# Performance work log

Hardware: AMD Instinct MI355X
Metric: run time of the kernel (lower is better)

## Reference

```python
import jax, jax.numpy as jnp
import numpy as np

TEMPERATURE = 0.0005

def conv1d(x, w, b):
    # x: [B,Cin,T], w: [Cout,Cin,K], 'same' padding as ConvNorm (pad=(K-1)//2)
    pad = (w.shape[-1] - 1) // 2
    y = jax.lax.conv_general_dilated(x, w, window_strides=(1,), padding=[(pad, pad)],
                                     dimension_numbers=('NCH', 'OIH', 'NCH'))
    return y + b[None, :, None]

def setup_inputs() -> dict:
    key = jax.random.key(0)
    ks = jax.random.split(key, 20)
    B, C_MEL, C_TXT, C_ATT, T1, T2 = 32, 80, 512, 80, 1600, 400
    s = 0.02
    return {
        'queries': jax.random.normal(ks[0], (B, C_MEL, T1), jnp.float32),
        'keys': jax.random.normal(ks[1], (B, C_TXT, T2), jnp.float32),
        'mask': jax.random.randint(ks[2], (B, T2, 1), 0, 2).astype(bool),
        'attn_prior': jax.random.uniform(ks[3], (B, T1, T2), jnp.float32),
        'speaker_embed': jax.random.normal(ks[4], (B, C_TXT), jnp.float32),
        # key_proj: Conv(512->1024,k3) -> ReLU -> Conv(1024->80,k1)
        'Wk1': jax.random.normal(ks[5], (C_TXT * 2, C_TXT, 3)) * s,
        'bk1': jax.random.normal(ks[6], (C_TXT * 2,)) * s,
        'Wk2': jax.random.normal(ks[7], (C_ATT, C_TXT * 2, 1)) * s,
        'bk2': jax.random.normal(ks[8], (C_ATT,)) * s,
        # query_proj: Conv(80->160,k3) -> ReLU -> Conv(160->80,k1) -> ReLU -> Conv(80->80,k1)
        'Wq1': jax.random.normal(ks[9], (C_MEL * 2, C_MEL, 3)) * s,
        'bq1': jax.random.normal(ks[10], (C_MEL * 2,)) * s,
        'Wq2': jax.random.normal(ks[11], (C_MEL, C_MEL * 2, 1)) * s,
        'bq2': jax.random.normal(ks[12], (C_MEL,)) * s,
        'Wq3': jax.random.normal(ks[13], (C_ATT, C_MEL, 1)) * s,
        'bq3': jax.random.normal(ks[14], (C_ATT,)) * s,
        # speaker projections (multi_speaker=True)
        'Wks': jax.random.normal(ks[15], (C_TXT, C_TXT)) * s,
        'bks': jax.random.normal(ks[16], (C_TXT,)) * s,
        'Wqs': jax.random.normal(ks[17], (C_MEL, C_TXT)) * s,
        'bqs': jax.random.normal(ks[18], (C_MEL,)) * s,
    }

def reference(queries, keys, mask, attn_prior, speaker_embed,
              Wk1, bk1, Wk2, bk2, Wq1, bq1, Wq2, bq2, Wq3, bq3,
              Wks, bks, Wqs, bqs):
    # speaker conditioning: Linear(spk) broadcast over time, added channelwise
    keys = keys + (speaker_embed @ Wks.T + bks)[:, :, None]
    queries = queries + (speaker_embed @ Wqs.T + bqs)[:, :, None]
    # projections
    k = jax.nn.relu(conv1d(keys, Wk1, bk1))
    k = conv1d(k, Wk2, bk2)                      # [B, C_att, T2]
    q = jax.nn.relu(conv1d(queries, Wq1, bq1))
    q = jax.nn.relu(conv1d(q, Wq2, bq2))
    q = conv1d(q, Wq3, bq3)                      # [B, C_att, T1]
    # -temp * sum_c (q-k)^2 == -temp * (||q||^2 + ||k||^2 - 2 q.k)
    q2 = jnp.sum(q * q, axis=1)                  # [B, T1]
    k2 = jnp.sum(k * k, axis=1)                  # [B, T2]
    qk = jnp.einsum('bct,bcs->bts', q, k)        # [B, T1, T2]
    attn = -TEMPERATURE * (q2[:, :, None] + k2[:, None, :] - 2.0 * qk)
    attn = attn[:, None]                         # [B, 1, T1, T2]
    attn = jax.nn.log_softmax(attn, axis=3) + jnp.log(attn_prior[:, None] + 1e-8)
    attn_logprob = attn
    m = jnp.transpose(mask, (0, 2, 1))[:, :, None, :]  # [B,1,1,T2]
    attn = jnp.where(m, -jnp.inf, attn)
    attn = jax.nn.softmax(attn, axis=3)
    return attn, attn_logprob
```

## Files before the change

### kernel.cpp

```cpp
#include <hip/hip_runtime.h>
#include <math.h>

#define TEMP 0.0005f
#define B_    32
#define CMEL  80
#define CTXT  512
#define T1_   1600
#define T2_   400

typedef short short8 __attribute__((ext_vector_type(8)));
typedef float f32x4 __attribute__((ext_vector_type(4)));

__device__ inline unsigned short f2bf(float f) {
    unsigned u = __float_as_uint(f);
    u += 0x7FFF + ((u >> 16) & 1);
    return (unsigned short)(u >> 16);
}
__device__ inline unsigned pack2(float a, float b) {
    return (unsigned)f2bf(a) | ((unsigned)f2bf(b) << 16);
}
__device__ inline float bf2f(unsigned short v) { return __uint_as_float(((unsigned)v) << 16); }

__global__ void bias_kernel(const float* __restrict__ se,
                            const float* __restrict__ Wks, const float* __restrict__ bks,
                            const float* __restrict__ Wqs, const float* __restrict__ bqs,
                            float* __restrict__ kb, float* __restrict__ qb) {
    int tid = blockIdx.x * blockDim.x + threadIdx.x;
    const int nk = B_ * CTXT;
    if (tid < nk) {
        int b = tid / CTXT, c = tid % CTXT;
        const float4* s4 = reinterpret_cast<const float4*>(se + b * CTXT);
        const float4* w4 = reinterpret_cast<const float4*>(Wks + (size_t)c * CTXT);
        float acc = bks[c];
        #pragma unroll 4
        for (int j = 0; j < CTXT / 4; ++j) {
            float4 a = s4[j], w = w4[j];
            acc += a.x * w.x + a.y * w.y + a.z * w.z + a.w * w.w;
        }
        kb[tid] = acc;
    } else if (tid < nk + B_ * CMEL) {
        int t = tid - nk;
        int b = t / CMEL, c = t % CMEL;
        const float4* s4 = reinterpret_cast<const float4*>(se + b * CTXT);
        const float4* w4 = reinterpret_cast<const float4*>(Wqs + (size_t)c * CTXT);
        float acc = bqs[c];
        #pragma unroll 4
        for (int j = 0; j < CTXT / 4; ++j) {
            float4 a = s4[j], w = w4[j];
            acc += a.x * w.x + a.y * w.y + a.z * w.z + a.w * w.w;
        }
        qb[t] = acc;
    }
}

__global__ void cast_weights_kernel(
        const float* __restrict__ Wk1, const float* __restrict__ Wk2,
        const float* __restrict__ Wq1, const float* __restrict__ Wq2,
        const float* __restrict__ Wq3,
        unsigned short* __restrict__ Ab1, unsigned short* __restrict__ A2,
        unsigned short* __restrict__ A3, unsigned short* __restrict__ A4,
        unsigned short* __restrict__ A5) {
    int e = blockIdx.x * 256 + threadIdx.x;
    const int n1 = 1572864, n2 = 81920, n3 = 46080, n4 = 12800, n5 = 7680;
    if (e < n1) {
        int co = e / 1536, rem = e - co * 1536;
        int dt = rem >> 9, ci = rem & 511;
        Ab1[e] = f2bf(Wk1[((size_t)co * 512 + ci) * 3 + dt]);
    } else if ((e -= n1) < n2) {
        A2[e] = f2bf(Wk2[e]);
    } else if ((e -= n2) < n3) {
        int co = e / 288, rem = e - co * 288;
        int dt = rem / 96, cc = rem - dt * 96;
        A3[e] = (cc < 80) ? f2bf(Wq1[((size_t)co * 80 + cc) * 3 + dt]) : 0;
    } else if ((e -= n3) < n4) {
        A4[e] = f2bf(Wq2[e]);
    } else if ((e -= n4) < n5) {
        int co = e / 96, cc = e - co * 96;
        A5[e] = (cc < 80) ? f2bf(Wq3[co * 80 + cc]) : 0;
    }
}

__global__ void castXk_kernel(const float* __restrict__ keys, const float* __restrict__ kb,
                              unsigned short* __restrict__ Xt) {
    __shared__ float tile[64][65];
    const int b = blockIdx.z;
    const int row0 = blockIdx.x * 64;
    const int ci0 = blockIdx.y * 64;
    const int tid = threadIdx.x;
    #pragma unroll
    for (int i = 0; i < 16; ++i) {
        int linear = i * 256 + tid;
        int ci_l = linear >> 6, t_l = linear & 63;
        int t = row0 + t_l - 1;
        float v = 0.f;
        if (t >= 0 && t < 400)
            v = keys[((size_t)b * 512 + ci0 + ci_l) * 400 + t] + kb[b * 512 + ci0 + ci_l];
        tile[t_l][ci_l] = v;
    }
    __syncthreads();
    #pragma unroll
    for (int i = 0; i < 16; ++i) {
        int linear = i * 256 + tid;
        int t_l = linear >> 6, ci_l = linear & 63;
        int row = row0 + t_l;
        if (row < 456)
            Xt[((size_t)b * 456 + row) * 512 + ci0 + ci_l] = f2bf(tile[t_l][ci_l]);
    }
}

__global__ __launch_bounds__(256) void castXq_kernel(
        const float* __restrict__ q, const float* __restrict__ qb,
        unsigned short* __restrict__ Xq1) {
    __shared__ float tile[80][65];
    const int b = blockIdx.y;
    const int t0 = blockIdx.x * 64;
    const int tid = threadIdx.x;
    if (t0 == 0 && tid < 48)
        ((unsigned*)(Xq1 + (size_t)b * 1602 * 96))[tid] = 0u;
    if (t0 == 1536 && tid < 48)
        ((unsigned*)(Xq1 + ((size_t)b * 1602 + 1601) * 96))[tid] = 0u;
    {
        int tl = tid & 63, c0 = tid >> 6;
        for (int c = c0; c < 80; c += 4)
            tile[c][tl] = q[((size_t)b * 80 + c) * 1600 + t0 + tl] + qb[b * 80 + c];
    }
    __syncthreads();
    int row = tid >> 2, cg = tid & 3;
    int t = t0 + row;
    unsigned* orow = (unsigned*)(Xq1 + ((size_t)b * 1602 + t + 1) * 96 + cg * 24);
    #pragma unroll
    for (int jj = 0; jj < 12; ++jj) {
        int c0 = cg * 24 + jj * 2, c1 = c0 + 1;
        float f0 = (c0 < 80) ? tile[c0][row] : 0.f;
        float f1 = (c1 < 80) ? tile[c1][row] : 0.f;
        orow[jj] = pack2(f0, f1);
    }
}

__global__ __launch_bounds__(256) void conv1k_mfma(
        const unsigned short* __restrict__ Ab, const unsigned short* __restrict__ Xt,
        const float* __restrict__ bias, unsigned short* __restrict__ k1c) {
    __shared__ short As[3 * 128 * 40];
    __shared__ short Xs[66 * 40];
    const int b = blockIdx.z;
    const int co0 = blockIdx.y * 128;
    const int t0 = blockIdx.x * 64;
    const int tid = threadIdx.x;
    const int lane = tid & 63, w = tid >> 6;
    const int wm = w >> 1, wn = w & 1;
    const int l15 = lane & 15, quad = lane >> 4;
    f32x4 acc[4][2];
    #pragma unroll
    for (int mt = 0; mt < 4; ++mt)
        #pragma unroll
        for (int nt = 0; nt < 2; ++nt)
            acc[mt][nt] = (f32x4){0.f, 0.f, 0.f, 0.f};

    for (int ci0 = 0; ci0 < 512; ci0 += 32) {
        __syncthreads();
        #pragma unroll
        for (int i = 0; i < 6; ++i) {
            int linear = i * 256 + tid;
            int dt = linear >> 9;
            int rem = linear & 511;
            int r = rem >> 2, c16 = rem & 3;
            int4 v = *(const int4*)(Ab + (size_t)(co0 + r) * 1536 + dt * 512 + ci0 + c16 * 8);
            *(int4*)(As + (dt * 128 + r) * 40 + c16 * 8) = v;
        }
        #pragma unroll
        for (int i = 0; i < 2; ++i) {
            int c = i * 256 + tid;
            if (c < 264) {
                int row = c >> 2, c16 = c & 3;
                int4 v = *(const int4*)(Xt + ((size_t)b * 456 + t0 + row) * 512 + ci0 + c16 * 8);
                *(int4*)(Xs + row * 40 + c16 * 8) = v;
            }
        }
        __syncthreads();
        #pragma unroll
        for (int dt = 0; dt < 3; ++dt) {
            short8 af[4], bfr[2];
            #pragma unroll
            for (int mt = 0; mt < 4; ++mt)
                af[mt] = *(const short8*)(As + (dt * 128 + wm * 64 + mt * 16 + l15) * 40 + quad * 8);
            #pragma unroll
            for (int nt = 0; nt < 2; ++nt)
                bfr[nt] = *(const short8*)(Xs + (wn * 32 + nt * 16 + l15 + dt) * 40 + quad * 8);
            #pragma unroll
            for (int mt = 0; mt < 4; ++mt)
                #pragma unroll
                for (int nt = 0; nt < 2; ++nt)
                    acc[mt][nt] = __builtin_amdgcn_mfma_f32_16x16x32_bf16(af[mt], bfr[nt], acc[mt][nt], 0, 0, 0);
        }
    }
    #pragma unroll
    for (int mt = 0; mt < 4; ++mt) {
        int cob = co0 + wm * 64 + mt * 16 + quad * 4;
        float bv[4];
        #pragma unroll
        for (int r = 0; r < 4; ++r) bv[r] = bias[cob + r];
        #pragma unroll
        for (int nt = 0; nt < 2; ++nt) {
            int t = t0 + wn * 32 + nt * 16 + l15;
            if (t >= 400) continue;
            float v0 = fmaxf(acc[mt][nt][0] + bv[0], 0.f);
            float v1 = fmaxf(acc[mt][nt][1] + bv[1], 0.f);
            float v2 = fmaxf(acc[mt][nt][2] + bv[2], 0.f);
            float v3 = fmaxf(acc[mt][nt][3] + bv[3], 0.f);
            uint2 p;
            p.x = pack2(v0, v1);
            p.y = pack2(v2, v3);
            *(uint2*)(k1c + ((size_t)b * 400 + t) * 1024 + cob) = p;
        }
    }
}

template<int MT, int NKC, int DTC, bool RELU, int OMODE, int INW, int OUTW, int N, int NR>
__global__ __launch_bounds__(256) void gemm_cl(
        const unsigned short* __restrict__ A, const unsigned short* __restrict__ X,
        const float* __restrict__ bias, unsigned short* __restrict__ out) {
    const int b = blockIdx.y;
    const int tid = threadIdx.x;
    const int lane = tid & 63, w = tid >> 6;
    const int l15 = lane & 15, quad = lane >> 4;
    const int s = blockIdx.x * 64 + w * 16 + l15;
    const int srow = (s < N) ? s : (N - 1);
    const unsigned short* xb = X + (size_t)b * NR * INW;

    f32x4 acc[MT];
    #pragma unroll
    for (int mt = 0; mt < MT; ++mt) acc[mt] = (f32x4){0.f, 0.f, 0.f, 0.f};

    #pragma unroll
    for (int kc = 0; kc < NKC; ++kc) {
        const int dt = DTC ? (kc / DTC) : 0;
        const int koff = DTC ? ((kc - dt * DTC) * 32) : (kc * 32);
        short8 bfr = *(const short8*)(xb + (size_t)(srow + dt) * INW + koff + quad * 8);
        #pragma unroll
        for (int mt = 0; mt < MT; ++mt) {
            short8 af = *(const short8*)(A + (size_t)(mt * 16 + l15) * (NKC * 32) + kc * 32 + quad * 8);
            acc[mt] = __builtin_amdgcn_mfma_f32_16x16x32_bf16(af, bfr, acc[mt], 0, 0, 0);
        }
    }
    if (s >= N) return;

    float v[MT][4];
    float ss = 0.f;
    #pragma unroll
    for (int mt = 0; mt < MT; ++mt) {
        #pragma unroll
        for (int r = 0; r < 4; ++r) {
            float x = acc[mt][r] + bias[mt * 16 + quad * 4 + r];
            if (RELU) x = fmaxf(x, 0.f);
            v[mt][r] = x;
            if (OMODE >= 2) ss += x * x;
        }
    }
    if (OMODE >= 2) {
        ss += __shfl_xor(ss, 16, 64);
        ss += __shfl_xor(ss, 32, 64);
    }
    unsigned short* orow = out + ((size_t)b * N + s) * OUTW;
    #pragma unroll
    for (int mt = 0; mt < MT; ++mt) {
        uint2 p;
        p.x = pack2(v[mt][0], v[mt][1]);
        p.y = pack2(v[mt][2], v[mt][3]);
        *(uint2*)(orow + mt * 16 + quad * 4) = p;
    }
    if (OMODE == 1 && quad == 0) {
        uint4 z = {0u, 0u, 0u, 0u};
        *(uint4*)(orow + 80) = z;
        *(uint4*)(orow + 88) = z;
    }
    if (OMODE >= 2 && quad == 0) {
        float e80 = (OMODE == 2) ? (-0.5f * ss) : 1.0f;
        float e81 = (OMODE == 2) ? 1.0f : (-0.5f * ss);
        uint4 z0 = {pack2(e80, e81), 0u, 0u, 0u};
        uint4 z1 = {0u, 0u, 0u, 0u};
        *(uint4*)(orow + 80) = z0;
        *(uint4*)(orow + 88) = z1;
    }
}

__global__ __launch_bounds__(64) void attn_logits_kernel(
        const unsigned short* __restrict__ qT, const unsigned short* __restrict__ kT,
        unsigned short* __restrict__ lgt) {
    const int b = blockIdx.y;
    const int t10 = blockIdx.x * 16;
    const int lane = threadIdx.x;
    const int l15 = lane & 15, quad = lane >> 4;

    const unsigned short* qrow = qT + ((size_t)b * T1_ + t10 + l15) * 96;
    short8 af[3];
    #pragma unroll
    for (int kc = 0; kc < 3; ++kc)
        af[kc] = *(const short8*)(qrow + kc * 32 + quad * 8);

    f32x4 acc[25];
    #pragma unroll
    for (int ns = 0; ns < 25; ++ns) acc[ns] = (f32x4){0.f, 0.f, 0.f, 0.f};
    const unsigned short* kbase = kT + (size_t)b * T2_ * 96 + l15 * 96 + quad * 8;
    #pragma unroll
    for (int ns = 0; ns < 25; ++ns) {
        #pragma unroll
        for (int kc = 0; kc < 3; ++kc) {
            short8 bf = *(const short8*)(kbase + ns * 16 * 96 + kc * 32);
            acc[ns] = __builtin_amdgcn_mfma_f32_16x16x32_bf16(af[kc], bf, acc[ns], 0, 0, 0);
        }
    }
    const float K2T = 2.0f * TEMP;
    #pragma unroll
    for (int r = 0; r < 4; ++r) {
        unsigned short* orow = lgt + ((size_t)b * T1_ + t10 + quad * 4 + r) * T2_;
        #pragma unroll
        for (int ns = 0; ns < 25; ++ns)
            orow[ns * 16 + l15] = f2bf(K2T * acc[ns][r]);
    }
}

__global__ __launch_bounds__(256) void softmax_kernel(
        const unsigned short* __restrict__ lgt, const int* __restrict__ mask,
        const float* __restrict__ prior,
        float* __restrict__ attn_out, float* __restrict__ lp_out) {
    const int b = blockIdx.y;
    const int t1 = blockIdx.x * 4 + (threadIdx.x >> 6);
    const int lane = threadIdx.x & 63;
    const unsigned short* lrow = lgt + ((size_t)b * T1_ + t1) * T2_;
    const float* prow = prior + ((size_t)b * T1_ + t1) * T2_;
    const int* mrow = mask + b * T2_;

    float l[7], pe[7], kp[7];
    #pragma unroll
    for (int j = 0; j < 7; ++j) {
        int s = lane + 64 * j;
        bool v = (j < 6) || (lane < 16);
        l[j]  = v ? bf2f(lrow[s]) : -1e30f;
        pe[j] = v ? (prow[s] + 1e-8f) : 1.f;
        kp[j] = (v && !mrow[v ? s : 0]) ? 1.f : 0.f;
    }
    float m = l[0];
    #pragma unroll
    for (int j = 1; j < 7; ++j) m = fmaxf(m, l[j]);
    #pragma unroll
    for (int off = 1; off <= 32; off <<= 1) m = fmaxf(m, __shfl_xor(m, off, 64));
    float e1[7];
    float sum = 0.f;
    #pragma unroll
    for (int j = 0; j < 7; ++j) { float e = __expf(l[j] - m); e1[j] = e; sum += e; }
    #pragma unroll
    for (int off = 1; off <= 32; off <<= 1) sum += __shfl_xor(sum, off, 64);
    const float lse = m + __logf(sum);

    float u[7];
    float sum2 = 0.f;
    #pragma unroll
    for (int j = 0; j < 7; ++j) {
        float uu = e1[j] * pe[j] * kp[j];
        u[j] = uu;
        sum2 += uu;
    }
    #pragma unroll
    for (int off = 1; off <= 32; off <<= 1) sum2 += __shfl_xor(sum2, off, 64);
    const float inv = 1.f / sum2;

    float* lpr = lp_out + ((size_t)b * T1_ + t1) * T2_;
    float* atr = attn_out + ((size_t)b * T1_ + t1) * T2_;
    #pragma unroll
    for (int j = 0; j < 7; ++j) {
        int s = lane + 64 * j;
        bool v = (j < 6) || (lane < 16);
        if (v) {
            lpr[s] = l[j] - lse + __logf(pe[j]);
            atr[s] = u[j] * inv;
        }
    }
}

extern "C" void kernel_launch(void* const* d_in, const int* in_sizes, int n_in,
                              void* d_out, int out_size, void* d_ws, size_t ws_size,
                              hipStream_t stream) {
    const float* queries = (const float*)d_in[0];
    const float* keys    = (const float*)d_in[1];
    const int*   mask    = (const int*)d_in[2];
    const float* prior   = (const float*)d_in[3];
    const float* se      = (const float*)d_in[4];
    const float* Wk1 = (const float*)d_in[5];
    const float* bk1 = (const float*)d_in[6];
    const float* Wk2 = (const float*)d_in[7];
    const float* bk2 = (const float*)d_in[8];
    const float* Wq1 = (const float*)d_in[9];
    const float* bq1 = (const float*)d_in[10];
    const float* Wq2 = (const float*)d_in[11];
    const float* bq2 = (const float*)d_in[12];
    const float* Wq3 = (const float*)d_in[13];
    const float* bq3 = (const float*)d_in[14];
    const float* Wks = (const float*)d_in[15];
    const float* bks = (const float*)d_in[16];
    const float* Wqs = (const float*)d_in[17];
    const float* bqs = (const float*)d_in[18];

    float* ws = (float*)d_ws;
    float* kb = ws;
    float* qb = ws + 16384;
    unsigned short* Ab1 = (unsigned short*)(ws + 18944);
    unsigned short* A2  = (unsigned short*)(ws + 805376);
    unsigned short* A3  = (unsigned short*)(ws + 846336);
    unsigned short* A4  = (unsigned short*)(ws + 869376);
    unsigned short* A5  = (unsigned short*)(ws + 875776);
    unsigned short* qT  = (unsigned short*)(ws + 879616);
    unsigned short* kT  = (unsigned short*)(ws + 3337216);
    const size_t D = 3951616;
    unsigned short* Xk  = (unsigned short*)(ws + D);
    unsigned short* k1c = (unsigned short*)(ws + D + 3735552);
    unsigned short* Xq1 = (unsigned short*)(ws + D);
    unsigned short* Xq2 = (unsigned short*)(ws + D + 2460672);
    unsigned short* Xq3 = (unsigned short*)(ws + D);
    unsigned short* lgt = (unsigned short*)(ws + D);

    float* attn_out = (float*)d_out;
    float* lp_out   = attn_out + (size_t)B_ * T1_ * T2_;

    bias_kernel<<<dim3(74), dim3(256), 0, stream>>>(se, Wks, bks, Wqs, bqs, kb, qb);
    cast_weights_kernel<<<dim3(6724), dim3(256), 0, stream>>>(Wk1, Wk2, Wq1, Wq2, Wq3,
                                                              Ab1, A2, A3, A4, A5);
    castXk_kernel<<<dim3(8, 8, 32), dim3(256), 0, stream>>>(keys, kb, Xk);
    conv1k_mfma<<<dim3(7, 8, 32), dim3(256), 0, stream>>>(Ab1, Xk, bk1, k1c);
    gemm_cl<5, 32, 0, false, 2, 1024, 96, 400, 400>
        <<<dim3(7, 32), 256, 0, stream>>>(A2, k1c, bk2, kT);
    castXq_kernel<<<dim3(25, 32), dim3(256), 0, stream>>>(queries, qb, Xq1);
    gemm_cl<10, 9, 3, true, 0, 96, 160, 1600, 1602>
        <<<dim3(25, 32), 256, 0, stream>>>(A3, Xq1, bq1, Xq2);
    gemm_cl<5, 5, 0, true, 1, 160, 96, 1600, 1600>
        <<<dim3(25, 32), 256, 0, stream>>>(A4, Xq2, bq2, Xq3);
    gemm_cl<5, 3, 0, false, 3, 96, 96, 1600, 1600>
        <<<dim3(25, 32), 256, 0, stream>>>(A5, Xq3, bq3, qT);
    attn_logits_kernel<<<dim3(100, 32), dim3(64), 0, stream>>>(qT, kT, lgt);
    softmax_kernel<<<dim3(400, 32), dim3(256), 0, stream>>>(lgt, mask, prior, attn_out, lp_out);
}
```

Measured before the change: 519.8 us.

## Fuse attention logits with softmax, prefetch conv tiles, split-K key GEMM, merge prep kernels

The attention-logit MFMA kernel and the softmax kernel become one kernel. Log-softmax, prior multiply, masking and normalisation now run in registers on the MFMA accumulators, so the bf16 logits no longer round-trip through global memory. The k3 key conv now prefetches the next global tile into registers while the current one is computed, the key k1 GEMM uses a split-K kernel with an LDS reduction across 4 waves for more parallelism, and the bias and weight-cast kernels are merged into one launch. In the fused kernel, prior reads and output writes are strided per row (16-wide per quad), which may coalesce worse than the old row-wise softmax.

Measured after the change: 924.9 us. 1.78x slower.

```diff
diff --git a/kernel.cpp b/kernel.cpp
--- a/kernel.cpp
+++ b/kernel.cpp
@@ -21,46 +21,46 @@
 }
 __device__ inline float bf2f(unsigned short v) { return __uint_as_float(((unsigned)v) << 16); }
 
-__global__ void bias_kernel(const float* __restrict__ se,
+__global__ void prep_kernel(const float* __restrict__ se,
                             const float* __restrict__ Wks, const float* __restrict__ bks,
                             const float* __restrict__ Wqs, const float* __restrict__ bqs,
-                            float* __restrict__ kb, float* __restrict__ qb) {
-    int tid = blockIdx.x * blockDim.x + threadIdx.x;
-    const int nk = B_ * CTXT;
-    if (tid < nk) {
-        int b = tid / CTXT, c = tid % CTXT;
-        const float4* s4 = reinterpret_cast<const float4*>(se + b * CTXT);
-        const float4* w4 = reinterpret_cast<const float4*>(Wks + (size_t)c * CTXT);
-        float acc = bks[c];
-        #pragma unroll 4
-        for (int j = 0; j < CTXT / 4; ++j) {
-            float4 a = s4[j], w = w4[j];
-            acc += a.x * w.x + a.y * w.y + a.z * w.z + a.w * w.w;
-        }
-        kb[tid] = acc;
-    } else if (tid < nk + B_ * CMEL) {
-        int t = tid - nk;
-        int b = t / CMEL, c = t % CMEL;
-        const float4* s4 = reinterpret_cast<const float4*>(se + b * CTXT);
-        const float4* w4 = reinterpret_cast<const float4*>(Wqs + (size_t)c * CTXT);
-        float acc = bqs[c];
-        #pragma unroll 4
-        for (int j = 0; j < CTXT / 4; ++j) {
-            float4 a = s4[j], w = w4[j];
-            acc += a.x * w.x + a.y * w.y + a.z * w.z + a.w * w.w;
-        }
-        qb[t] = acc;
-    }
-}
-
-__global__ void cast_weights_kernel(
-        const float* __restrict__ Wk1, const float* __restrict__ Wk2,
-        const float* __restrict__ Wq1, const float* __restrict__ Wq2,
-        const float* __restrict__ Wq3,
-        unsigned short* __restrict__ Ab1, unsigned short* __restrict__ A2,
-        unsigned short* __restrict__ A3, unsigned short* __restrict__ A4,
-        unsigned short* __restrict__ A5) {
-    int e = blockIdx.x * 256 + threadIdx.x;
+                            float* __restrict__ kb, float* __restrict__ qb,
+                            const float* __restrict__ Wk1, const float* __restrict__ Wk2,
+                            const float* __restrict__ Wq1, const float* __restrict__ Wq2,
+                            const float* __restrict__ Wq3,
+                            unsigned short* __restrict__ Ab1, unsigned short* __restrict__ A2,
+                            unsigned short* __restrict__ A3, unsigned short* __restrict__ A4,
+                            unsigned short* __restrict__ A5) {
+    if (blockIdx.x < 74) {
+        int tid = blockIdx.x * blockDim.x + threadIdx.x;
+        const int nk = B_ * CTXT;
+        if (tid < nk) {
+            int b = tid / CTXT, c = tid % CTXT;
+            const float4* s4 = reinterpret_cast<const float4*>(se + b * CTXT);
+            const float4* w4 = reinterpret_cast<const float4*>(Wks + (size_t)c * CTXT);
+            float acc = bks[c];
+            #pragma unroll 4
+            for (int j = 0; j < CTXT / 4; ++j) {
+                float4 a = s4[j], w = w4[j];
+                acc += a.x * w.x + a.y * w.y + a.z * w.z + a.w * w.w;
+            }
+            kb[tid] = acc;
+        } else if (tid < nk + B_ * CMEL) {
+            int t = tid - nk;
+            int b = t / CMEL, c = t % CMEL;
+            const float4* s4 = reinterpret_cast<const float4*>(se + b * CTXT);
+            const float4* w4 = reinterpret_cast<const float4*>(Wqs + (size_t)c * CTXT);
+            float acc = bqs[c];
+            #pragma unroll 4
+            for (int j = 0; j < CTXT / 4; ++j) {
+                float4 a = s4[j], w = w4[j];
+                acc += a.x * w.x + a.y * w.y + a.z * w.z + a.w * w.w;
+            }
+            qb[t] = acc;
+        }
+        return;
+    }
+    int e = (blockIdx.x - 74) * 256 + threadIdx.x;
     const int n1 = 1572864, n2 = 81920, n3 = 46080, n4 = 12800, n5 = 7680;
     if (e < n1) {
         int co = e / 1536, rem = e - co * 1536;
@@ -156,27 +156,52 @@
         for (int nt = 0; nt < 2; ++nt)
             acc[mt][nt] = (f32x4){0.f, 0.f, 0.f, 0.f};
 
+    int4 pA[6];
+    int4 pX[2];
+
+    int a_dt[6], a_r[6], a_c16[6];
+    #pragma unroll
+    for (int i = 0; i < 6; ++i) {
+        int linear = i * 256 + tid;
+        a_dt[i] = linear >> 9;
+        int rem = linear & 511;
+        a_r[i] = rem >> 2; a_c16[i] = rem & 3;
+    }
+    int x_row[2], x_c16[2]; bool x_ok[2];
+    #pragma unroll
+    for (int i = 0; i < 2; ++i) {
+        int c = i * 256 + tid;
+        x_ok[i] = (c < 264);
+        x_row[i] = c >> 2; x_c16[i] = c & 3;
+    }
+
+    #pragma unroll
+    for (int i = 0; i < 6; ++i)
+        pA[i] = *(const int4*)(Ab + (size_t)(co0 + a_r[i]) * 1536 + a_dt[i] * 512 + a_c16[i] * 8);
+    #pragma unroll
+    for (int i = 0; i < 2; ++i)
+        if (x_ok[i])
+            pX[i] = *(const int4*)(Xt + ((size_t)b * 456 + t0 + x_row[i]) * 512 + x_c16[i] * 8);
+
     for (int ci0 = 0; ci0 < 512; ci0 += 32) {
+        #pragma unroll
+        for (int i = 0; i < 6; ++i)
+            *(int4*)(As + (a_dt[i] * 128 + a_r[i]) * 40 + a_c16[i] * 8) = pA[i];
+        #pragma unroll
+        for (int i = 0; i < 2; ++i)
+            if (x_ok[i])
+                *(int4*)(Xs + x_row[i] * 40 + x_c16[i] * 8) = pX[i];
         __syncthreads();
-        #pragma unroll
-        for (int i = 0; i < 6; ++i) {
-            int linear = i * 256 + tid;
-            int dt = linear >> 9;
-            int rem = linear & 511;
-            int r = rem >> 2, c16 = rem & 3;
-            int4 v = *(const int4*)(Ab + (size_t)(co0 + r) * 1536 + dt * 512 + ci0 + c16 * 8);
-            *(int4*)(As + (dt * 128 + r) * 40 + c16 * 8) = v;
-        }
-        #pragma unroll
-        for (int i = 0; i < 2; ++i) {
-            int c = i * 256 + tid;
-            if (c < 264) {
-                int row = c >> 2, c16 = c & 3;
-                int4 v = *(const int4*)(Xt + ((size_t)b * 456 + t0 + row) * 512 + ci0 + c16 * 8);
-                *(int4*)(Xs + row * 40 + c16 * 8) = v;
-            }
-        }
-        __syncthreads();
+        if (ci0 + 32 < 512) {
+            int cn = ci0 + 32;
+            #pragma unroll
+            for (int i = 0; i < 6; ++i)
+                pA[i] = *(const int4*)(Ab + (size_t)(co0 + a_r[i]) * 1536 + a_dt[i] * 512 + cn + a_c16[i] * 8);
+            #pragma unroll
+            for (int i = 0; i < 2; ++i)
+                if (x_ok[i])
+                    pX[i] = *(const int4*)(Xt + ((size_t)b * 456 + t0 + x_row[i]) * 512 + cn + x_c16[i] * 8);
+        }
         #pragma unroll
         for (int dt = 0; dt < 3; ++dt) {
             short8 af[4], bfr[2];
@@ -192,6 +217,7 @@
                 for (int nt = 0; nt < 2; ++nt)
                     acc[mt][nt] = __builtin_amdgcn_mfma_f32_16x16x32_bf16(af[mt], bfr[nt], acc[mt][nt], 0, 0, 0);
         }
+        __syncthreads();
     }
     #pragma unroll
     for (int mt = 0; mt < 4; ++mt) {
@@ -283,13 +309,81 @@
     }
 }
 
-__global__ __launch_bounds__(64) void attn_logits_kernel(
+__global__ __launch_bounds__(256) void gemm_k2_kernel(
+        const unsigned short* __restrict__ A, const unsigned short* __restrict__ X,
+        const float* __restrict__ bias, unsigned short* __restrict__ out) {
+    __shared__ float red[3][64][21];
+    const int b = blockIdx.y;
+    const int tid = threadIdx.x, lane = tid & 63, w = tid >> 6;
+    const int l15 = lane & 15, quad = lane >> 4;
+    const int s = blockIdx.x * 16 + l15;
+    const unsigned short* xb = X + ((size_t)b * 400 + s) * 1024 + quad * 8;
+    f32x4 acc[5];
+    #pragma unroll
+    for (int mt = 0; mt < 5; ++mt) acc[mt] = (f32x4){0.f, 0.f, 0.f, 0.f};
+    #pragma unroll
+    for (int kk = 0; kk < 8; ++kk) {
+        int kc = w * 8 + kk;
+        short8 bfr = *(const short8*)(xb + kc * 32);
+        #pragma unroll
+        for (int mt = 0; mt < 5; ++mt) {
+            short8 af = *(const short8*)(A + (size_t)(mt * 16 + l15) * 1024 + kc * 32 + quad * 8);
+            acc[mt] = __builtin_amdgcn_mfma_f32_16x16x32_bf16(af, bfr, acc[mt], 0, 0, 0);
+        }
+    }
+    if (w > 0) {
+        #pragma unroll
+        for (int mt = 0; mt < 5; ++mt)
+            #pragma unroll
+            for (int r = 0; r < 4; ++r)
+                red[w - 1][lane][mt * 4 + r] = acc[mt][r];
+    }
+    __syncthreads();
+    if (w != 0) return;
+    #pragma unroll
+    for (int wv = 0; wv < 3; ++wv)
+        #pragma unroll
+        for (int mt = 0; mt < 5; ++mt)
+            #pragma unroll
+            for (int r = 0; r < 4; ++r)
+                acc[mt][r] += red[wv][lane][mt * 4 + r];
+    float v[5][4];
+    float ss = 0.f;
+    #pragma unroll
+    for (int mt = 0; mt < 5; ++mt)
+        #pragma unroll
+        for (int r = 0; r < 4; ++r) {
+            float x = acc[mt][r] + bias[mt * 16 + quad * 4 + r];
+            v[mt][r] = x;
+            ss += x * x;
+        }
+    ss += __shfl_xor(ss, 16, 64);
+    ss += __shfl_xor(ss, 32, 64);
+    unsigned short* orow = out + ((size_t)b * 400 + s) * 96;
+    #pragma unroll
+    for (int mt = 0; mt < 5; ++mt) {
+        uint2 p;
+        p.x = pack2(v[mt][0], v[mt][1]);
+        p.y = pack2(v[mt][2], v[mt][3]);
+        *(uint2*)(orow + mt * 16 + quad * 4) = p;
+    }
+    if (quad == 0) {
+        uint4 z0 = {pack2(-0.5f * ss, 1.0f), 0u, 0u, 0u};
+        uint4 z1 = {0u, 0u, 0u, 0u};
+        *(uint4*)(orow + 80) = z0;
+        *(uint4*)(orow + 88) = z1;
+    }
+}
+
+__global__ __launch_bounds__(256) void attn_fused_kernel(
         const unsigned short* __restrict__ qT, const unsigned short* __restrict__ kT,
-        unsigned short* __restrict__ lgt) {
+        const int* __restrict__ mask, const float* __restrict__ prior,
+        float* __restrict__ attn_out, float* __restrict__ lp_out) {
     const int b = blockIdx.y;
-    const int t10 = blockIdx.x * 16;
-    const int lane = threadIdx.x;
+    const int w = threadIdx.x >> 6;
+    const int lane = threadIdx.x & 63;
     const int l15 = lane & 15, quad = lane >> 4;
+    const int t10 = blockIdx.x * 64 + w * 16;
 
     const unsigned short* qrow = qT + ((size_t)b * T1_ + t10 + l15) * 96;
     short8 af[3];
@@ -309,70 +403,71 @@
             acc[ns] = __builtin_amdgcn_mfma_f32_16x16x32_bf16(af[kc], bf, acc[ns], 0, 0, 0);
         }
     }
+
     const float K2T = 2.0f * TEMP;
-    #pragma unroll
-    for (int r = 0; r < 4; ++r) {
-        unsigned short* orow = lgt + ((size_t)b * T1_ + t10 + quad * 4 + r) * T2_;
-        #pragma unroll
-        for (int ns = 0; ns < 25; ++ns)
-            orow[ns * 16 + l15] = f2bf(K2T * acc[ns][r]);
-    }
-}
-
-__global__ __launch_bounds__(256) void softmax_kernel(
-        const unsigned short* __restrict__ lgt, const int* __restrict__ mask,
-        const float* __restrict__ prior,
-        float* __restrict__ attn_out, float* __restrict__ lp_out) {
-    const int b = blockIdx.y;
-    const int t1 = blockIdx.x * 4 + (threadIdx.x >> 6);
-    const int lane = threadIdx.x & 63;
-    const unsigned short* lrow = lgt + ((size_t)b * T1_ + t1) * T2_;
-    const float* prow = prior + ((size_t)b * T1_ + t1) * T2_;
+    float M[4] = {-1e30f, -1e30f, -1e30f, -1e30f};
+    #pragma unroll
+    for (int ns = 0; ns < 25; ++ns)
+        #pragma unroll
+        for (int r = 0; r < 4; ++r) M[r] = fmaxf(M[r], K2T * acc[ns][r]);
+    #pragma unroll
+    for (int off = 1; off <= 8; off <<= 1)
+        #pragma unroll
+        for (int r = 0; r < 4; ++r) M[r] = fmaxf(M[r], __shfl_xor(M[r], off, 64));
+
+    float sum1[4] = {0.f, 0.f, 0.f, 0.f};
+    #pragma unroll
+    for (int ns = 0; ns < 25; ++ns)
+        #pragma unroll
+        for (int r = 0; r < 4; ++r) {
+            float e = __expf(K2T * acc[ns][r] - M[r]);
+            acc[ns][r] = e;
+            sum1[r] += e;
+        }
+    #pragma unroll
+    for (int off = 1; off <= 8; off <<= 1)
+        #pragma unroll
+        for (int r = 0; r < 4; ++r) sum1[r] += __shfl_xor(sum1[r], off, 64);
+    float mlse[4];
+    #pragma unroll
+    for (int r = 0; r < 4; ++r) mlse[r] = -__logf(sum1[r]);
+
     const int* mrow = mask + b * T2_;
-
-    float l[7], pe[7], kp[7];
-    #pragma unroll
-    for (int j = 0; j < 7; ++j) {
-        int s = lane + 64 * j;
-        bool v = (j < 6) || (lane < 16);
-        l[j]  = v ? bf2f(lrow[s]) : -1e30f;
-        pe[j] = v ? (prow[s] + 1e-8f) : 1.f;
-        kp[j] = (v && !mrow[v ? s : 0]) ? 1.f : 0.f;
-    }
-    float m = l[0];
-    #pragma unroll
-    for (int j = 1; j < 7; ++j) m = fmaxf(m, l[j]);
-    #pragma unroll
-    for (int off = 1; off <= 32; off <<= 1) m = fmaxf(m, __shfl_xor(m, off, 64));
-    float e1[7];
-    float sum = 0.f;
-    #pragma unroll
-    for (int j = 0; j < 7; ++j) { float e = __expf(l[j] - m); e1[j] = e; sum += e; }
-    #pragma unroll
-    for (int off = 1; off <= 32; off <<= 1) sum += __shfl_xor(sum, off, 64);
-    const float lse = m + __logf(sum);
-
-    float u[7];
-    float sum2 = 0.f;
-    #pragma unroll
-    for (int j = 0; j < 7; ++j) {
-        float uu = e1[j] * pe[j] * kp[j];
-        u[j] = uu;
-        sum2 += uu;
-    }
-    #pragma unroll
-    for (int off = 1; off <= 32; off <<= 1) sum2 += __shfl_xor(sum2, off, 64);
-    const float inv = 1.f / sum2;
-
-    float* lpr = lp_out + ((size_t)b * T1_ + t1) * T2_;
-    float* atr = attn_out + ((size_t)b * T1_ + t1) * T2_;
-    #pragma unroll
-    for (int j = 0; j < 7; ++j) {
-        int s = lane + 64 * j;
-        bool v = (j < 6) || (lane < 16);
-        if (v) {
-            lpr[s] = l[j] - lse + __logf(pe[j]);
-            atr[s] = u[j] * inv;
+    const float* pb = prior + ((size_t)b * T1_ + t10) * T2_;
+    float sum2[4] = {0.f, 0.f, 0.f, 0.f};
+    unsigned mbits = 0;
+    #pragma unroll
+    for (int ns = 0; ns < 25; ++ns) {
+        int s = ns * 16 + l15;
+        unsigned mk = mrow[s] ? 1u : 0u;
+        mbits |= (mk << ns);
+        #pragma unroll
+        for (int r = 0; r < 4; ++r) {
+            float pe = pb[(size_t)(quad * 4 + r) * T2_ + s] + 1e-8f;
+            float u = acc[ns][r] * pe;
+            acc[ns][r] = u;
+            sum2[r] += mk ? 0.f : u;
+        }
+    }
+    #pragma unroll
+    for (int off = 1; off <= 8; off <<= 1)
+        #pragma unroll
+        for (int r = 0; r < 4; ++r) sum2[r] += __shfl_xor(sum2[r], off, 64);
+    float inv[4];
+    #pragma unroll
+    for (int r = 0; r < 4; ++r) inv[r] = 1.f / sum2[r];
+
+    float* ab = attn_out + ((size_t)b * T1_ + t10) * T2_;
+    float* lb = lp_out + ((size_t)b * T1_ + t10) * T2_;
+    #pragma unroll
+    for (int ns = 0; ns < 25; ++ns) {
+        int s = ns * 16 + l15;
+        float km = ((mbits >> ns) & 1u) ? 0.f : 1.f;
+        #pragma unroll
+        for (int r = 0; r < 4; ++r) {
+            size_t o = (size_t)(quad * 4 + r) * T2_ + s;
+            ab[o] = acc[ns][r] * km * inv[r];
+            lb[o] = __logf(acc[ns][r]) + mlse[r];
         }
     }
 }
@@ -416,18 +511,16 @@
     unsigned short* Xq1 = (unsigned short*)(ws + D);
     unsigned short* Xq2 = (unsigned short*)(ws + D + 2460672);
     unsigned short* Xq3 = (unsigned short*)(ws + D);
-    unsigned short* lgt = (unsigned short*)(ws + D);
 
     float* attn_out = (float*)d_out;
     float* lp_out   = attn_out + (size_t)B_ * T1_ * T2_;
 
-    bias_kernel<<<dim3(74), dim3(256), 0, stream>>>(se, Wks, bks, Wqs, bqs, kb, qb);
-    cast_weights_kernel<<<dim3(6724), dim3(256), 0, stream>>>(Wk1, Wk2, Wq1, Wq2, Wq3,
-                                                              Ab1, A2, A3, A4, A5);
+    prep_kernel<<<dim3(6798), dim3(256), 0, stream>>>(se, Wks, bks, Wqs, bqs, kb, qb,
+                                                      Wk1, Wk2, Wq1, Wq2, Wq3,
+                                                      Ab1, A2, A3, A4, A5);
     castXk_kernel<<<dim3(8, 8, 32), dim3(256), 0, stream>>>(keys, kb, Xk);
     conv1k_mfma<<<dim3(7, 8, 32), dim3(256), 0, stream>>>(Ab1, Xk, bk1, k1c);
-    gemm_cl<5, 32, 0, false, 2, 1024, 96, 400, 400>
-        <<<dim3(7, 32), 256, 0, stream>>>(A2, k1c, bk2, kT);
+    gemm_k2_kernel<<<dim3(25, 32), 256, 0, stream>>>(A2, k1c, bk2, kT);
     castXq_kernel<<<dim3(25, 32), dim3(256), 0, stream>>>(queries, qb, Xq1);
     gemm_cl<10, 9, 3, true, 0, 96, 160, 1600, 1602>
         <<<dim3(25, 32), 256, 0, stream>>>(A3, Xq1, bq1, Xq2);
@@ -435,6 +528,6 @@
         <<<dim3(25, 32), 256, 0, stream>>>(A4, Xq2, bq2, Xq3);
     gemm_cl<5, 3, 0, false, 3, 96, 96, 1600, 1600>
         <<<dim3(25, 32), 256, 0, stream>>>(A5, Xq3, bq3, qT);
-    attn_logits_kernel<<<dim3(100, 32), dim3(64), 0, stream>>>(qT, kT, lgt);
-    softmax_kernel<<<dim3(400, 32), dim3(256), 0, stream>>>(lgt, mask, prior, attn_out, lp_out);
-}
+    attn_fused_kernel<<<dim3(25, 32), dim3(256), 0, stream>>>(qT, kT, mask, prior,
+                                                              attn_out, lp_out);
+}
```
